# Kernel tuning notes

Measured on AMD Instinct MI355X. Metric: run time of the kernel, lower is better.

The kernel has to match this reference:

```python
import jax, jax.numpy as jnp
import numpy as np
from jax import lax

CL, IL = 128, 64            # context_length, inst_length (globals in original)
PC, CH1, CH2, CH3 = 64, 128, 256, 256
CK1 = CK2 = CK3 = 3
F1, OUT = 400, 1
B = 4096
C3_OUT = CH3 * (CL - 1 - CK1 - CK2 - CK3 + 3)   # 256*121 = 30976
F1_IN = C3_OUT + CL * IL                        # 39168


def _uni(k, shape, fan_in):
    s = 1.0 / np.sqrt(fan_in)
    return jax.random.uniform(k, shape, jnp.float32, -s, s)


def setup_inputs() -> dict:
    key = jax.random.key(0)
    ks = jax.random.split(key, 14)
    x = jax.random.normal(ks[0], (B, CL * IL), jnp.float32)
    Wp = _uni(ks[1], (PC, IL, 2), IL * 2); bp = _uni(ks[2], (PC,), IL * 2)
    W1 = _uni(ks[3], (CH1, PC, CK1), PC * CK1); b1 = _uni(ks[4], (CH1,), PC * CK1)
    W2 = _uni(ks[5], (CH2, CH1, CK2), CH1 * CK2); b2 = _uni(ks[6], (CH2,), CH1 * CK2)
    W3 = _uni(ks[7], (CH3, CH2, CK3), CH2 * CK3); b3 = _uni(ks[8], (CH3,), CH2 * CK3)
    Wf1 = _uni(ks[9], (F1, F1_IN), F1_IN); bf1 = _uni(ks[10], (F1,), F1_IN)
    Wf2 = _uni(ks[11], (OUT, F1), F1); bf2 = _uni(ks[12], (OUT,), F1)
    return dict(x=x, Wp=Wp, bp=bp, W1=W1, b1=b1, W2=W2, b2=b2,
                W3=W3, b3=b3, Wf1=Wf1, bf1=bf1, Wf2=Wf2, bf2=bf2)


def _conv1d(h, w, b):
    # h: [B,C,L], w: [O,C,K], valid conv, stride 1
    return lax.conv_general_dilated(h, w, (1,), 'VALID',
                                    dimension_numbers=('NCH', 'OIH', 'NCH')) + b[None, :, None]


def reference(x, Wp, bp, W1, b1, W2, b2, W3, b3, Wf1, bf1, Wf2, bf2):
    b = x.shape[0]
    xt = x.reshape(b, CL, IL).transpose(0, 2, 1)          # [B, IL, CL]
    # Fused pairwise convp: original loops i=1..CL-1 over k=2 Conv1d on
    # (x[:,:,0], x[:,:,i]); equivalent to one shared term + one batched matmul.
    base = jnp.einsum('pc,bc->bp', Wp[:, :, 0], xt[:, :, 0])        # [B, PC]
    rest = jnp.einsum('pc,bci->bpi', Wp[:, :, 1], xt[:, :, 1:])     # [B, PC, CL-1]
    h = jax.nn.relu(base[:, :, None] + rest + bp[None, :, None])
    h = jax.nn.relu(_conv1d(h, W1, b1))
    h = jax.nn.relu(_conv1d(h, W2, b2))
    h = jax.nn.relu(_conv1d(h, W3, b3))
    h = h.reshape(b, C3_OUT)
    h = jnp.concatenate([h, xt.reshape(b, IL * CL)], axis=1)        # [B, F1_IN]
    h = jax.nn.relu(h @ Wf1.T + bf1)
    return h @ Wf2.T + bf2
```

## Files before the change

### kernel.cpp

```cpp
#include <hip/hip_runtime.h>


typedef __attribute__((ext_vector_type(8))) short bf16x8;
typedef __attribute__((ext_vector_type(4))) float f32x4;
typedef __attribute__((ext_vector_type(8))) unsigned short u16x8;
typedef __attribute__((ext_vector_type(4))) unsigned short u16x4;

#define DEVINL __device__ __forceinline__

DEVINL unsigned short f2bf(float f) {
  unsigned u = __builtin_bit_cast(unsigned, f);
  return (unsigned short)((u + 0x7fffu + ((u >> 16) & 1u)) >> 16);
}
DEVINL float bf2f(unsigned short h) {
  return __builtin_bit_cast(float, ((unsigned)h) << 16);
}
DEVINL f32x4 mfma16(bf16x8 a, bf16x8 b, f32x4 c) {
  return __builtin_amdgcn_mfma_f32_16x16x32_bf16(a, b, c, 0, 0, 0);
}
DEVINL float relu(float v) { return v > 0.f ? v : 0.f; }
DEVINL int sxg(int r, int c, int sh) {
  return (r << sh) + (((c >> 3) ^ (r & 7)) << 3) + (c & 7);
}

constexpr int NB = 4096;

__global__ __launch_bounds__(256) void k_prep_w(
    const float* __restrict__ Wp, const float* __restrict__ W1,
    const float* __restrict__ W2, const float* __restrict__ W3,
    unsigned short* __restrict__ wp1r, unsigned short* __restrict__ wp0r,
    unsigned short* __restrict__ w1p, unsigned short* __restrict__ w2p,
    unsigned short* __restrict__ w3p) {
  int idx = blockIdx.x * 256 + threadIdx.x;
  if (idx < 4096) {
    int p = idx >> 6, i = idx & 63;
    wp1r[p * 64 + i] = f2bf(Wp[(p * 64 + i) * 2 + 1]);
    wp0r[i * 64 + p] = f2bf(Wp[(p * 64 + i) * 2 + 0]);
    return;
  }
  idx -= 4096;
  if (idx < 24576) {
    int f = idx >> 9, l = (idx >> 3) & 63, e = idx & 7;
    int mt = f & 7, t = f >> 3, ks = t & 1, k = t >> 1;
    int o = mt * 16 + (l & 15), c = ks * 32 + (l >> 4) * 8 + e;
    w1p[idx] = f2bf(W1[(o * 64 + c) * 3 + k]);
    return;
  }
  idx -= 24576;
  if (idx < 98304) {
    int f = idx >> 9, l = (idx >> 3) & 63, e = idx & 7;
    int mt = f & 15, t = f >> 4, ks = t & 3, k = t >> 2;
    int o = mt * 16 + (l & 15), c = ks * 32 + (l >> 4) * 8 + e;
    w2p[idx] = f2bf(W2[(o * 128 + c) * 3 + k]);
    return;
  }
  idx -= 98304;
  if (idx < 196608) {
    int f = idx >> 9, l = (idx >> 3) & 63, e = idx & 7;
    int mt = f & 15, t = f >> 4, ks = t & 7, k = t >> 3;
    int o = mt * 16 + (l & 15), c = ks * 32 + (l >> 4) * 8 + e;
    w3p[idx] = f2bf(W3[(o * 256 + c) * 3 + k]);
  }
}

__global__ __launch_bounds__(256) void k_prep_wf1(const float* __restrict__ wf1,
                                                  unsigned short* __restrict__ wf1r) {
  extern __shared__ unsigned short tls[];
  const int m = blockIdx.x / 5, q = blockIdx.x % 5, tid = threadIdx.x;
  unsigned short* dst = wf1r + (size_t)m * 39168;
  if (q < 4) {
    const float* src = wf1 + (size_t)m * 39168 + q * 7744;
    for (int idx = tid; idx < 7744; idx += 256) {
      int o = idx / 121, l = idx - o * 121;
      tls[o * 132 + l] = f2bf(src[idx]);
    }
    __syncthreads();
    for (int idx = tid; idx < 7744; idx += 256) {
      int l = idx >> 6, o = idx & 63;
      dst[l * 256 + q * 64 + o] = tls[o * 132 + l];
    }
  } else {
    const float* src = wf1 + (size_t)m * 39168 + 30976;
    for (int idx = tid; idx < 8192; idx += 256) {
      int il = idx >> 7, cl = idx & 127;
      tls[cl * 66 + il] = f2bf(src[idx]);
    }
    __syncthreads();
    for (int idx = tid; idx < 8192; idx += 256) {
      int cl = idx >> 6, il = idx & 63;
      dst[30976 + idx] = tls[cl * 66 + il];
    }
  }
}

template <int CIN, int COUT, int LIN, int LOUT, int SSHI, int SSHO, bool TOGLB>
DEVINL void conv16(const unsigned short* in_lds,
                   const unsigned short* __restrict__ wpack,
                   const float* __restrict__ bias, unsigned short* out_lds,
                   unsigned short* h3, int b, int lane, int wv) {
  constexpr int KS = CIN / 32;
  constexpr int MT = COUT / 16;
  constexpr int MPW = MT / 4;
  const int lr = lane & 15, lq = lane >> 4;
  const int wm = wv >> 1, wn = wv & 1;
  f32x4 acc[MPW][4];
#pragma unroll
  for (int mi = 0; mi < MPW; ++mi)
#pragma unroll
    for (int ni = 0; ni < 4; ++ni) acc[mi][ni] = (f32x4){0.f, 0.f, 0.f, 0.f};
#pragma unroll
  for (int k = 0; k < 3; ++k)
#pragma unroll
    for (int ks = 0; ks < KS; ++ks) {
      bf16x8 a[MPW];
#pragma unroll
      for (int mi = 0; mi < MPW; ++mi)
        a[mi] = *(const bf16x8*)(wpack +
                                 (((k * KS + ks) * MT + wm * MPW + mi) << 9) +
                                 lane * 8);
      const int col = ks * 32 + lq * 8;
#pragma unroll
      for (int ni = 0; ni < 4; ++ni) {
        int l = (wn * 4 + ni) * 16 + lr + k;
        if (l > LIN - 1) l = LIN - 1;
        bf16x8 bb = *(const bf16x8*)(in_lds + sxg(l, col, SSHI));
#pragma unroll
        for (int mi = 0; mi < MPW; ++mi)
          acc[mi][ni] = mfma16(a[mi], bb, acc[mi][ni]);
      }
    }
#pragma unroll
  for (int mi = 0; mi < MPW; ++mi) {
    const int o0 = (wm * MPW + mi) * 16 + lq * 4;
    const f32x4 bi = *(const f32x4*)(bias + o0);
#pragma unroll
    for (int ni = 0; ni < 4; ++ni) {
      const int l = (wn * 4 + ni) * 16 + lr;
      if (l < LOUT) {
        u16x4 pk;
#pragma unroll
        for (int r = 0; r < 4; ++r) pk[r] = f2bf(relu(acc[mi][ni][r] + bi[r]));
        if constexpr (TOGLB)
          *(u16x4*)(h3 + ((size_t)b * LOUT + l) * COUT + o0) = pk;
        else
          *(u16x4*)(out_lds + sxg(l, o0, SSHO)) = pk;
      }
    }
  }
}

__global__ __launch_bounds__(512) void k_front(
    const float* __restrict__ x, const unsigned short* __restrict__ wp0r,
    const float* __restrict__ bp, const unsigned short* __restrict__ wp1r,
    const unsigned short* __restrict__ w1p, const float* __restrict__ b1,
    const unsigned short* __restrict__ w2p, const float* __restrict__ b2,
    const unsigned short* __restrict__ w3p, const float* __restrict__ b3,
    unsigned short* __restrict__ h3) {
  extern __shared__ unsigned short lds[];
  unsigned short* xs = lds;
  unsigned short* h1s = lds;
  unsigned short* h0s = lds + 16000;
  unsigned short* h2s = lds + 16000;
  __shared__ float pbase[8][64];
  __shared__ float basel[64];
  const int b = blockIdx.x, tid = threadIdx.x;
  const int lane = tid & 63, wv = tid >> 6, lq = lane >> 4, lr = lane & 15;
  const float* xb = x + (size_t)b * 8192;

  for (int idx = tid * 4; idx < 8192; idx += 2048) {
    f32x4 v = *(const f32x4*)(xb + idx);
    int c = idx >> 6, i = idx & 63;
    u16x4 pk;
#pragma unroll
    for (int r = 0; r < 4; ++r) pk[r] = f2bf(v[r]);
    *(u16x4*)(xs + sxg(c, i, 6)) = pk;
  }
  __syncthreads();

  {
    int p = tid & 63, q = tid >> 6;
    float s = 0.f;
#pragma unroll
    for (int t = 0; t < 8; ++t) {
      int i = q * 8 + t;
      s += bf2f(wp0r[i * 64 + p]) * bf2f(xs[i]);
    }
    pbase[q][p] = s;
  }
  __syncthreads();
  if (tid < 64) {
    float s = bp[tid];
#pragma unroll
    for (int q = 0; q < 8; ++q) s += pbase[q][tid];
    basel[tid] = s;
  }
  __syncthreads();

  {
    const int mt = wv & 3, nh = wv >> 2;
    f32x4 acc[4];
#pragma unroll
    for (int t = 0; t < 4; ++t) acc[t] = (f32x4){0.f, 0.f, 0.f, 0.f};
#pragma unroll
    for (int s = 0; s < 2; ++s) {
      bf16x8 a = *(const bf16x8*)(wp1r + (mt * 16 + lr) * 64 + s * 32 + lq * 8);
#pragma unroll
      for (int t = 0; t < 4; ++t) {
        int j = (nh * 4 + t) * 16 + lr;
        int row = j + 1 > 127 ? 127 : j + 1;
        bf16x8 bb = *(const bf16x8*)(xs + sxg(row, s * 32 + lq * 8, 6));
        acc[t] = mfma16(a, bb, acc[t]);
      }
    }
    const int m0 = mt * 16 + lq * 4;
    f32x4 bl;
#pragma unroll
    for (int r = 0; r < 4; ++r) bl[r] = basel[m0 + r];
#pragma unroll
    for (int t = 0; t < 4; ++t) {
      int j = (nh * 4 + t) * 16 + lr;
      if (j < 127) {
        u16x4 pk;
#pragma unroll
        for (int r = 0; r < 4; ++r) pk[r] = f2bf(relu(acc[t][r] + bl[r]));
        *(u16x4*)(h0s + sxg(j, m0, 6)) = pk;
      }
    }
  }
  __syncthreads();

  conv16<64, 128, 127, 125, 6, 7, false>(h0s, w1p, b1, h1s, nullptr, b, lane, wv);
  __syncthreads();
  conv16<128, 256, 125, 123, 7, 8, false>(h1s, w2p, b2, h2s, nullptr, b, lane, wv);
  __syncthreads();
  conv16<256, 256, 123, 121, 8, 0, true>(h2s, w3p, b3, nullptr, h3, b, lane, wv);
}

__global__ __launch_bounds__(512) void k_fc1(const unsigned short* __restrict__ h3,
                                             const float* __restrict__ x,
                                             const unsigned short* __restrict__ wf1r,
                                             float* __restrict__ fpart,
                                             int chunkN, int S) {
  __shared__ unsigned short lB[2][128 * 64];
  const int tid = threadIdx.x;
  const int lane = tid & 63, wv = tid >> 6, lq = lane >> 4, lr = lane & 15;
  const int slice = blockIdx.x % S;
  const int bbase = (blockIdx.x / S) * 128;
  const int per = 612 / S, rem = 612 % S;
  const int c0 = slice * per + (slice < rem ? slice : rem);
  const int c1 = c0 + per + (slice < rem ? 1 : 0);

  f32x4 acc[3][8], acc24;
#pragma unroll
  for (int mi = 0; mi < 3; ++mi)
#pragma unroll
    for (int nt = 0; nt < 8; ++nt) acc[mi][nt] = (f32x4){0.f, 0.f, 0.f, 0.f};
  acc24 = (f32x4){0.f, 0.f, 0.f, 0.f};

  const size_t arow0 = (size_t)((3 * wv + 0) * 16 + lr) * 39168;
  const size_t arow1 = (size_t)((3 * wv + 1) * 16 + lr) * 39168;
  const size_t arow2 = (size_t)((3 * wv + 2) * 16 + lr) * 39168;
  const size_t arow24 = (size_t)(384 + lr) * 39168;

  const int sn0 = tid >> 3, sch0 = tid & 7;
  const int sn1 = (tid + 512) >> 3, sch1 = tid & 7;
  const unsigned short* hrow0 = h3 + (size_t)(bbase + sn0) * 30976 + sch0 * 8;
  const unsigned short* hrow1 = h3 + (size_t)(bbase + sn1) * 30976 + sch1 * 8;
  const float* xrow0 = x + (size_t)(bbase + sn0) * 8192 + sch0 * 8;
  const float* xrow1 = x + (size_t)(bbase + sn1) * 8192 + sch1 * 8;
  const int woff0 = (sn0 << 6) + ((sch0 ^ (sn0 & 7)) << 3);
  const int woff1 = (sn1 << 6) + ((sch1 ^ (sn1 & 7)) << 3);

  u16x8 hv0, hv1;
  f32x4 xv00, xv01, xv10, xv11;
  bool isx;

#define FC1_GLOAD(KC)                                                     \
  {                                                                       \
    const int k0_ = (KC)*64;                                              \
    isx = (k0_ >= 30976);                                                 \
    if (!isx) {                                                           \
      hv0 = *(const u16x8*)(hrow0 + k0_);                                 \
      hv1 = *(const u16x8*)(hrow1 + k0_);                                 \
    } else {                                                              \
      xv00 = *(const f32x4*)(xrow0 + (k0_ - 30976));                      \
      xv01 = *(const f32x4*)(xrow0 + (k0_ - 30976) + 4);                  \
      xv10 = *(const f32x4*)(xrow1 + (k0_ - 30976));                      \
      xv11 = *(const f32x4*)(xrow1 + (k0_ - 30976) + 4);                  \
    }                                                                     \
  }
#define FC1_DSWRITE(BUF)                                                  \
  {                                                                       \
    if (isx) {                                                            \
      _Pragma("unroll") for (int r = 0; r < 4; ++r) {                     \
        hv0[r] = f2bf(xv00[r]);                                           \
        hv0[4 + r] = f2bf(xv01[r]);                                       \
        hv1[r] = f2bf(xv10[r]);                                           \
        hv1[4 + r] = f2bf(xv11[r]);                                       \
      }                                                                   \
    }                                                                     \
    *(u16x8*)(lB[BUF] + woff0) = hv0;                                     \
    *(u16x8*)(lB[BUF] + woff1) = hv1;                                     \
  }

  FC1_GLOAD(c0)
  FC1_DSWRITE(0)
  __syncthreads();

  for (int kc = c0; kc < c1; ++kc) {
    const int p = (kc - c0) & 1;
    const int k0 = kc * 64;
    const bool more = (kc + 1 < c1);
    if (more) FC1_GLOAD(kc + 1)

    bf16x8 aP[2][4];
#pragma unroll
    for (int win = 0; win < 2; ++win) {
      const int koff = k0 + win * 32 + lq * 8;
      aP[win][0] = *(const bf16x8*)(wf1r + arow0 + koff);
      aP[win][1] = *(const bf16x8*)(wf1r + arow1 + koff);
      aP[win][2] = *(const bf16x8*)(wf1r + arow2 + koff);
      aP[win][3] = *(const bf16x8*)(wf1r + arow24 + koff);
    }
#pragma unroll
    for (int win = 0; win < 2; ++win) {
      const int cloc = win * 32 + lq * 8;
#pragma unroll
      for (int nt = 0; nt < 8; ++nt) {
        const int n = nt * 16 + lr;
        bf16x8 bb = *(const bf16x8*)(lB[p] + sxg(n, cloc, 6));
        acc[0][nt] = mfma16(aP[win][0], bb, acc[0][nt]);
        acc[1][nt] = mfma16(aP[win][1], bb, acc[1][nt]);
        acc[2][nt] = mfma16(aP[win][2], bb, acc[2][nt]);
      }
      {
        const int n = wv * 16 + lr;
        bf16x8 bb = *(const bf16x8*)(lB[p] + sxg(n, cloc, 6));
        acc24 = mfma16(aP[win][3], bb, acc24);
      }
    }
    if (more) FC1_DSWRITE(p ^ 1)
    __syncthreads();
  }
#undef FC1_GLOAD
#undef FC1_DSWRITE

#pragma unroll
  for (int mi = 0; mi < 3; ++mi) {
    const int m0 = (3 * wv + mi) * 16 + lq * 4;
#pragma unroll
    for (int nt = 0; nt < 8; ++nt) {
      const int bb = bbase + nt * 16 + lr;
      *(f32x4*)(fpart + ((size_t)slice * chunkN + bb) * 400 + m0) = acc[mi][nt];
    }
  }
  {
    const int bb = bbase + wv * 16 + lr;
    *(f32x4*)(fpart + ((size_t)slice * chunkN + bb) * 400 + 384 + lq * 4) = acc24;
  }
}

__global__ __launch_bounds__(256) void k_fc1red(const float* __restrict__ fpart,
                                                const float* __restrict__ bf1,
                                                float* __restrict__ fc,
                                                int chunkN, int S) {
  int idx = blockIdx.x * 256 + threadIdx.x;
  if (idx >= chunkN * 400) return;
  int m = idx % 400;
  float s = bf1[m];
  size_t stride = (size_t)chunkN * 400;
#pragma unroll 4
  for (int sl = 0; sl < S; ++sl) s += fpart[(size_t)sl * stride + idx];
  fc[idx] = relu(s);
}

__global__ __launch_bounds__(256) void k_fc2(const float* __restrict__ fc,
                                             const float* __restrict__ wf2,
                                             const float* __restrict__ bf2,
                                             float* __restrict__ out) {
  int b = blockIdx.x * 4 + (threadIdx.x >> 6);
  int lane = threadIdx.x & 63;
  float s = 0.f;
  for (int m = lane; m < 400; m += 64) s += fc[(size_t)b * 400 + m] * wf2[m];
#pragma unroll
  for (int off = 32; off > 0; off >>= 1) s += __shfl_down(s, off, 64);
  if (lane == 0) out[b] = s + bf2[0];
}

extern "C" void kernel_launch(void* const* d_in, const int* in_sizes, int n_in,
                              void* d_out, int out_size, void* d_ws, size_t ws_size,
                              hipStream_t stream) {
  const float* x = (const float*)d_in[0];
  const float* Wp = (const float*)d_in[1];
  const float* bp = (const float*)d_in[2];
  const float* W1 = (const float*)d_in[3];
  const float* b1 = (const float*)d_in[4];
  const float* W2 = (const float*)d_in[5];
  const float* b2 = (const float*)d_in[6];
  const float* W3 = (const float*)d_in[7];
  const float* b3 = (const float*)d_in[8];
  const float* Wf1 = (const float*)d_in[9];
  const float* bf1 = (const float*)d_in[10];
  const float* Wf2 = (const float*)d_in[11];
  const float* bf2 = (const float*)d_in[12];
  float* out = (float*)d_out;

  const size_t fixed =
      8192 + 8192 + 49152 + 196608 + 393216 + 400ULL * 39168 * 2;
  const int S = 16;
  static const int cand[3] = {2048, 1024, 512};
  int chunkN = 512;
  for (int i = 0; i < 3; ++i) {
    size_t cn = cand[i];
    size_t need = fixed + cn * 61952ULL + (size_t)S * cn * 1600ULL + cn * 1600ULL;
    if (need <= ws_size) {
      chunkN = cand[i];
      break;
    }
  }
  const int nchunk = NB / chunkN;

  char* ws = (char*)d_ws;
  size_t off = 0;
  unsigned short* h3c = (unsigned short*)(ws + off);
  off += (size_t)chunkN * 61952ULL;
  float* fpart = (float*)(ws + off);
  off += (size_t)S * chunkN * 1600ULL;
  float* fc = (float*)(ws + off);
  off += (size_t)chunkN * 1600ULL;
  unsigned short* wp1r = (unsigned short*)(ws + off);
  off += 8192;
  unsigned short* wp0r = (unsigned short*)(ws + off);
  off += 8192;
  unsigned short* w1p = (unsigned short*)(ws + off);
  off += 49152;
  unsigned short* w2p = (unsigned short*)(ws + off);
  off += 196608;
  unsigned short* w3p = (unsigned short*)(ws + off);
  off += 393216;
  unsigned short* wf1r = (unsigned short*)(ws + off);

  k_prep_w<<<1264, 256, 0, stream>>>(Wp, W1, W2, W3, wp1r, wp0r, w1p, w2p, w3p);
  k_prep_wf1<<<2000, 256, 16896, stream>>>(Wf1, wf1r);

  for (int c = 0; c < nchunk; ++c) {
    const float* xc = x + (size_t)c * chunkN * 8192;
    k_front<<<chunkN, 512, 94976, stream>>>(xc, wp0r, bp, wp1r, w1p, b1, w2p,
                                            b2, w3p, b3, h3c);
    k_fc1<<<(chunkN / 128) * S, 512, 0, stream>>>(h3c, xc, wf1r, fpart, chunkN, S);
    k_fc1red<<<(chunkN * 400 + 255) / 256, 256, 0, stream>>>(fpart, bf1, fc,
                                                             chunkN, S);
    k_fc2<<<chunkN / 4, 256, 0, stream>>>(fc, Wf2, bf2, out + (size_t)c * chunkN);
  }
}
```

Baseline: 693.9 us.

## Halve fc1 batch tile to 64, add occupancy hints, use packed bf16 converts

The fc1 GEMM now processes 64 batch rows per block instead of 128. This halves the LDS tile and the accumulator registers and doubles the grid, with launch bounds asking for two blocks per CU. A-operand loads are moved inside the window loop so fewer registers stay live. The 400-row tail is now handled only by the first four waves, since the tile holds just four 16-row groups. Float-to-bf16 packing everywhere now uses the v_cvt_pk_bf16_f32 instruction instead of manual rounding. In exchange, each Wf1 A-fragment is reused over half as many batch columns, so weight traffic per output doubles.

```diff
diff --git a/kernel.cpp b/kernel.cpp
--- a/kernel.cpp
+++ b/kernel.cpp
@@ -5,6 +5,8 @@
 typedef __attribute__((ext_vector_type(4))) float f32x4;
 typedef __attribute__((ext_vector_type(8))) unsigned short u16x8;
 typedef __attribute__((ext_vector_type(4))) unsigned short u16x4;
+typedef __attribute__((ext_vector_type(2))) unsigned int u32x2;
+typedef __attribute__((ext_vector_type(4))) unsigned int u32x4;
 
 #define DEVINL __device__ __forceinline__
 
@@ -14,6 +16,11 @@
 }
 DEVINL float bf2f(unsigned short h) {
   return __builtin_bit_cast(float, ((unsigned)h) << 16);
+}
+DEVINL unsigned cvtpk(float lo, float hi) {
+  unsigned r;
+  asm("v_cvt_pk_bf16_f32 %0, %1, %2" : "=v"(r) : "v"(lo), "v"(hi));
+  return r;
 }
 DEVINL f32x4 mfma16(bf16x8 a, bf16x8 b, f32x4 c) {
   return __builtin_amdgcn_mfma_f32_16x16x32_bf16(a, b, c, 0, 0, 0);
@@ -137,19 +144,19 @@
     for (int ni = 0; ni < 4; ++ni) {
       const int l = (wn * 4 + ni) * 16 + lr;
       if (l < LOUT) {
-        u16x4 pk;
-#pragma unroll
-        for (int r = 0; r < 4; ++r) pk[r] = f2bf(relu(acc[mi][ni][r] + bi[r]));
+        u32x2 pk;
+        pk.x = cvtpk(relu(acc[mi][ni][0] + bi[0]), relu(acc[mi][ni][1] + bi[1]));
+        pk.y = cvtpk(relu(acc[mi][ni][2] + bi[2]), relu(acc[mi][ni][3] + bi[3]));
         if constexpr (TOGLB)
-          *(u16x4*)(h3 + ((size_t)b * LOUT + l) * COUT + o0) = pk;
+          *(u32x2*)(h3 + ((size_t)b * LOUT + l) * COUT + o0) = pk;
         else
-          *(u16x4*)(out_lds + sxg(l, o0, SSHO)) = pk;
-      }
-    }
-  }
-}
-
-__global__ __launch_bounds__(512) void k_front(
+          *(u32x2*)(out_lds + sxg(l, o0, SSHO)) = pk;
+      }
+    }
+  }
+}
+
+__global__ __launch_bounds__(512, 1) void k_front(
     const float* __restrict__ x, const unsigned short* __restrict__ wp0r,
     const float* __restrict__ bp, const unsigned short* __restrict__ wp1r,
     const unsigned short* __restrict__ w1p, const float* __restrict__ b1,
@@ -170,10 +177,10 @@
   for (int idx = tid * 4; idx < 8192; idx += 2048) {
     f32x4 v = *(const f32x4*)(xb + idx);
     int c = idx >> 6, i = idx & 63;
-    u16x4 pk;
-#pragma unroll
-    for (int r = 0; r < 4; ++r) pk[r] = f2bf(v[r]);
-    *(u16x4*)(xs + sxg(c, i, 6)) = pk;
+    u32x2 pk;
+    pk.x = cvtpk(v[0], v[1]);
+    pk.y = cvtpk(v[2], v[3]);
+    *(u32x2*)(xs + sxg(c, i, 6)) = pk;
   }
   __syncthreads();
 
@@ -220,10 +227,10 @@
     for (int t = 0; t < 4; ++t) {
       int j = (nh * 4 + t) * 16 + lr;
       if (j < 127) {
-        u16x4 pk;
-#pragma unroll
-        for (int r = 0; r < 4; ++r) pk[r] = f2bf(relu(acc[t][r] + bl[r]));
-        *(u16x4*)(h0s + sxg(j, m0, 6)) = pk;
+        u32x2 pk;
+        pk.x = cvtpk(relu(acc[t][0] + bl[0]), relu(acc[t][1] + bl[1]));
+        pk.y = cvtpk(relu(acc[t][2] + bl[2]), relu(acc[t][3] + bl[3]));
+        *(u32x2*)(h0s + sxg(j, m0, 6)) = pk;
       }
     }
   }
@@ -236,25 +243,24 @@
   conv16<256, 256, 123, 121, 8, 0, true>(h2s, w3p, b3, nullptr, h3, b, lane, wv);
 }
 
-__global__ __launch_bounds__(512) void k_fc1(const unsigned short* __restrict__ h3,
-                                             const float* __restrict__ x,
-                                             const unsigned short* __restrict__ wf1r,
-                                             float* __restrict__ fpart,
-                                             int chunkN, int S) {
-  __shared__ unsigned short lB[2][128 * 64];
+__global__ __launch_bounds__(512, 2) void k_fc1(
+    const unsigned short* __restrict__ h3, const float* __restrict__ x,
+    const unsigned short* __restrict__ wf1r, float* __restrict__ fpart,
+    int chunkN, int S) {
+  __shared__ unsigned short lB[2][64 * 64];
   const int tid = threadIdx.x;
   const int lane = tid & 63, wv = tid >> 6, lq = lane >> 4, lr = lane & 15;
   const int slice = blockIdx.x % S;
-  const int bbase = (blockIdx.x / S) * 128;
+  const int bbase = (blockIdx.x / S) * 64;
   const int per = 612 / S, rem = 612 % S;
   const int c0 = slice * per + (slice < rem ? slice : rem);
   const int c1 = c0 + per + (slice < rem ? 1 : 0);
 
-  f32x4 acc[3][8], acc24;
+  f32x4 acc[3][4], acc24;
 #pragma unroll
   for (int mi = 0; mi < 3; ++mi)
 #pragma unroll
-    for (int nt = 0; nt < 8; ++nt) acc[mi][nt] = (f32x4){0.f, 0.f, 0.f, 0.f};
+    for (int nt = 0; nt < 4; ++nt) acc[mi][nt] = (f32x4){0.f, 0.f, 0.f, 0.f};
   acc24 = (f32x4){0.f, 0.f, 0.f, 0.f};
 
   const size_t arow0 = (size_t)((3 * wv + 0) * 16 + lr) * 39168;
@@ -262,17 +268,13 @@
   const size_t arow2 = (size_t)((3 * wv + 2) * 16 + lr) * 39168;
   const size_t arow24 = (size_t)(384 + lr) * 39168;
 
-  const int sn0 = tid >> 3, sch0 = tid & 7;
-  const int sn1 = (tid + 512) >> 3, sch1 = tid & 7;
-  const unsigned short* hrow0 = h3 + (size_t)(bbase + sn0) * 30976 + sch0 * 8;
-  const unsigned short* hrow1 = h3 + (size_t)(bbase + sn1) * 30976 + sch1 * 8;
-  const float* xrow0 = x + (size_t)(bbase + sn0) * 8192 + sch0 * 8;
-  const float* xrow1 = x + (size_t)(bbase + sn1) * 8192 + sch1 * 8;
-  const int woff0 = (sn0 << 6) + ((sch0 ^ (sn0 & 7)) << 3);
-  const int woff1 = (sn1 << 6) + ((sch1 ^ (sn1 & 7)) << 3);
-
-  u16x8 hv0, hv1;
-  f32x4 xv00, xv01, xv10, xv11;
+  const int sn = tid >> 3, sch = tid & 7;
+  const unsigned short* hrow = h3 + (size_t)(bbase + sn) * 30976 + sch * 8;
+  const float* xrow = x + (size_t)(bbase + sn) * 8192 + sch * 8;
+  const int woff = (sn << 6) + ((sch ^ (sn & 7)) << 3);
+
+  u32x4 hv;
+  f32x4 xv0, xv1;
   bool isx;
 
 #define FC1_GLOAD(KC)                                                     \
@@ -280,27 +282,21 @@
     const int k0_ = (KC)*64;                                              \
     isx = (k0_ >= 30976);                                                 \
     if (!isx) {                                                           \
-      hv0 = *(const u16x8*)(hrow0 + k0_);                                 \
-      hv1 = *(const u16x8*)(hrow1 + k0_);                                 \
+      hv = *(const u32x4*)(hrow + k0_);                                   \
     } else {                                                              \
-      xv00 = *(const f32x4*)(xrow0 + (k0_ - 30976));                      \
-      xv01 = *(const f32x4*)(xrow0 + (k0_ - 30976) + 4);                  \
-      xv10 = *(const f32x4*)(xrow1 + (k0_ - 30976));                      \
-      xv11 = *(const f32x4*)(xrow1 + (k0_ - 30976) + 4);                  \
+      xv0 = *(const f32x4*)(xrow + (k0_ - 30976));                        \
+      xv1 = *(const f32x4*)(xrow + (k0_ - 30976) + 4);                    \
     }                                                                     \
   }
 #define FC1_DSWRITE(BUF)                                                  \
   {                                                                       \
     if (isx) {                                                            \
-      _Pragma("unroll") for (int r = 0; r < 4; ++r) {                     \
-        hv0[r] = f2bf(xv00[r]);                                           \
-        hv0[4 + r] = f2bf(xv01[r]);                                       \
-        hv1[r] = f2bf(xv10[r]);                                           \
-        hv1[4 + r] = f2bf(xv11[r]);                                       \
-      }                                                                   \
+      hv.x = cvtpk(xv0[0], xv0[1]);                                       \
+      hv.y = cvtpk(xv0[2], xv0[3]);                                       \
+      hv.z = cvtpk(xv1[0], xv1[1]);                                       \
+      hv.w = cvtpk(xv1[2], xv1[3]);                                       \
     }                                                                     \
-    *(u16x8*)(lB[BUF] + woff0) = hv0;                                     \
-    *(u16x8*)(lB[BUF] + woff1) = hv1;                                     \
+    *(u32x4*)(lB[BUF] + woff) = hv;                                       \
   }
 
   FC1_GLOAD(c0)
@@ -313,30 +309,26 @@
     const bool more = (kc + 1 < c1);
     if (more) FC1_GLOAD(kc + 1)
 
-    bf16x8 aP[2][4];
 #pragma unroll
     for (int win = 0; win < 2; ++win) {
       const int koff = k0 + win * 32 + lq * 8;
-      aP[win][0] = *(const bf16x8*)(wf1r + arow0 + koff);
-      aP[win][1] = *(const bf16x8*)(wf1r + arow1 + koff);
-      aP[win][2] = *(const bf16x8*)(wf1r + arow2 + koff);
-      aP[win][3] = *(const bf16x8*)(wf1r + arow24 + koff);
-    }
-#pragma unroll
-    for (int win = 0; win < 2; ++win) {
+      bf16x8 a0 = *(const bf16x8*)(wf1r + arow0 + koff);
+      bf16x8 a1 = *(const bf16x8*)(wf1r + arow1 + koff);
+      bf16x8 a2 = *(const bf16x8*)(wf1r + arow2 + koff);
       const int cloc = win * 32 + lq * 8;
 #pragma unroll
-      for (int nt = 0; nt < 8; ++nt) {
+      for (int nt = 0; nt < 4; ++nt) {
         const int n = nt * 16 + lr;
         bf16x8 bb = *(const bf16x8*)(lB[p] + sxg(n, cloc, 6));
-        acc[0][nt] = mfma16(aP[win][0], bb, acc[0][nt]);
-        acc[1][nt] = mfma16(aP[win][1], bb, acc[1][nt]);
-        acc[2][nt] = mfma16(aP[win][2], bb, acc[2][nt]);
-      }
-      {
+        acc[0][nt] = mfma16(a0, bb, acc[0][nt]);
+        acc[1][nt] = mfma16(a1, bb, acc[1][nt]);
+        acc[2][nt] = mfma16(a2, bb, acc[2][nt]);
+      }
+      if (wv < 4) {
+        bf16x8 a24 = *(const bf16x8*)(wf1r + arow24 + koff);
         const int n = wv * 16 + lr;
         bf16x8 bb = *(const bf16x8*)(lB[p] + sxg(n, cloc, 6));
-        acc24 = mfma16(aP[win][3], bb, acc24);
+        acc24 = mfma16(a24, bb, acc24);
       }
     }
     if (more) FC1_DSWRITE(p ^ 1)
@@ -349,12 +341,12 @@
   for (int mi = 0; mi < 3; ++mi) {
     const int m0 = (3 * wv + mi) * 16 + lq * 4;
 #pragma unroll
-    for (int nt = 0; nt < 8; ++nt) {
+    for (int nt = 0; nt < 4; ++nt) {
       const int bb = bbase + nt * 16 + lr;
       *(f32x4*)(fpart + ((size_t)slice * chunkN + bb) * 400 + m0) = acc[mi][nt];
     }
   }
-  {
+  if (wv < 4) {
     const int bb = bbase + wv * 16 + lr;
     *(f32x4*)(fpart + ((size_t)slice * chunkN + bb) * 400 + 384 + lq * 4) = acc24;
   }
@@ -447,7 +439,7 @@
     const float* xc = x + (size_t)c * chunkN * 8192;
     k_front<<<chunkN, 512, 94976, stream>>>(xc, wp0r, bp, wp1r, w1p, b1, w2p,
                                             b2, w3p, b3, h3c);
-    k_fc1<<<(chunkN / 128) * S, 512, 0, stream>>>(h3c, xc, wf1r, fpart, chunkN, S);
+    k_fc1<<<(chunkN / 64) * S, 512, 0, stream>>>(h3c, xc, wf1r, fpart, chunkN, S);
     k_fc1red<<<(chunkN * 400 + 255) / 256, 256, 0, stream>>>(fpart, bf1, fc,
                                                              chunkN, S);
     k_fc2<<<chunkN / 4, 256, 0, stream>>>(fc, Wf2, bf2, out + (size_t)c * chunkN);
```

New measurement: 717.9 us. +3.5%, slower.
